# Kernel tuning notes

Hardware: AMD Instinct MI355X
Metric: run time of the kernel (lower is better)

The kernel has to match this reference:

```python
import jax, jax.numpy as jnp
import numpy as np

B, T, C = 8, 1024, 384
L, H, D, F = 8, 16, 24, 1536
EPS = 1e-5

def _ln(x, g, b):
    m = jnp.mean(x, axis=-1, keepdims=True)
    v = jnp.mean(jnp.square(x - m), axis=-1, keepdims=True)
    return (x - m) * jax.lax.rsqrt(v + EPS) * g + b

def setup_inputs() -> dict:
    key = jax.random.key(0)
    ks = jax.random.split(key, 8)
    s = 0.02
    return {
        "idx": jax.random.uniform(ks[0], (B, T, C), jnp.float32),
        "pos_emb": jax.random.normal(ks[1], (T, C), jnp.float32) * s,
        "Wq": jax.random.normal(ks[2], (L, H, C, D), jnp.float32) * s,
        "Wk": jax.random.normal(ks[3], (L, H, C, D), jnp.float32) * s,
        "Wv": jax.random.normal(ks[4], (L, H, C, D), jnp.float32) * s,
        "Wo": jax.random.normal(ks[5], (L, C, C), jnp.float32) * s,
        "bo": jnp.zeros((L, C), jnp.float32),
        "ln1_g": jnp.ones((L, C), jnp.float32),
        "ln1_b": jnp.zeros((L, C), jnp.float32),
        "ln2_g": jnp.ones((L, C), jnp.float32),
        "ln2_b": jnp.zeros((L, C), jnp.float32),
        "W1": jax.random.normal(ks[6], (L, C, F), jnp.float32) * s,
        "b1": jnp.zeros((L, F), jnp.float32),
        "W2": jax.random.normal(ks[7], (L, F, C), jnp.float32) * s,
        "b2": jnp.zeros((L, C), jnp.float32),
        "lnf_g": jnp.ones((C,), jnp.float32),
        "lnf_b": jnp.zeros((C,), jnp.float32),
    }

def reference(idx, pos_emb, Wq, Wk, Wv, Wo, bo, ln1_g, ln1_b, ln2_g, ln2_b,
              W1, b1, W2, b2, lnf_g, lnf_b):
    Bc, Tc, Cc = idx.shape
    x = idx + pos_emb[:Tc]
    causal = jnp.tril(jnp.ones((Tc, Tc), bool))  # [T,T]
    scale = D ** -0.5
    for l in range(L):
        h = _ln(x, ln1_g[l], ln1_b[l])
        q = jnp.einsum('btc,hcd->bhtd', h, Wq[l])
        k = jnp.einsum('btc,hcd->bhtd', h, Wk[l])
        v = jnp.einsum('btc,hcd->bhtd', h, Wv[l])
        wei = jnp.einsum('bhtd,bhsd->bhts', q, k) * scale
        wei = jnp.where(causal, wei, -jnp.inf)
        wei = jax.nn.softmax(wei, axis=-1)
        o = jnp.einsum('bhts,bhsd->bhtd', wei, v)
        o = o.transpose(0, 2, 1, 3).reshape(Bc, Tc, H * D)
        x = x + o @ Wo[l] + bo[l]
        h2 = _ln(x, ln2_g[l], ln2_b[l])
        x = x + jax.nn.relu(h2 @ W1[l] + b1[l]) @ W2[l] + b2[l]
    x = _ln(x, lnf_g, lnf_b)
    return jax.nn.relu(x)  # MSE path with targets=None
```

## Files before the change

kernel.cpp:

```cpp
#include <hip/hip_runtime.h>

#define B_ 8
#define T_ 1024
#define C_ 384
#define L_ 8
#define H_ 16
#define D_ 24
#define F_ 1536
#define M_ 8192

using bf16x8 = __attribute__((ext_vector_type(8))) __bf16;
using f32x4  = __attribute__((ext_vector_type(4))) float;

__device__ __forceinline__ ushort f2b(float f) {
  union { float f; unsigned u; } cv; cv.f = f;
  unsigned u = cv.u;
  return (ushort)((u + 0x7FFFu + ((u >> 16) & 1u)) >> 16);
}
__device__ __forceinline__ ushort f2b_cvt(float f) {
  __bf16 h = (__bf16)f;
  return *(ushort*)&h;
}
__device__ __forceinline__ void gload_lds16(const void* g, void* l) {
  __builtin_amdgcn_global_load_lds((const __attribute__((address_space(1))) void*)g,
                                   (__attribute__((address_space(3))) void*)l, 16, 0, 0);
}

#define QSCL 0.29448870f

__global__ __launch_bounds__(256) void k_embed(const float* __restrict__ idx,
                                               const float* __restrict__ pos,
                                               float* __restrict__ x) {
  long i4 = ((long)blockIdx.x * 256 + threadIdx.x) * 4;
  float4 a = *(const float4*)(idx + i4);
  long p = i4 % (long)(T_ * C_);
  float4 b = *(const float4*)(pos + p);
  a.x += b.x; a.y += b.y; a.z += b.z; a.w += b.w;
  *(float4*)(x + i4) = a;
}

__global__ __launch_bounds__(256) void k_ln(const float* __restrict__ x,
                                            const float* __restrict__ g,
                                            const float* __restrict__ b,
                                            ushort* __restrict__ out) {
  int row  = blockIdx.x * 4 + (threadIdx.x >> 6);
  int lane = threadIdx.x & 63;
  const float* xr = x + (long)row * C_;
  float v[6]; float sum = 0.f;
#pragma unroll
  for (int i = 0; i < 3; ++i) {
    float2 t = *(const float2*)(xr + 2*(lane + 64*i));
    v[2*i] = t.x; v[2*i+1] = t.y; sum += t.x + t.y;
  }
#pragma unroll
  for (int m = 1; m < 64; m <<= 1) sum += __shfl_xor(sum, m);
  float mean = sum * (1.f / C_);
  float vs = 0.f;
#pragma unroll
  for (int i = 0; i < 6; ++i) { float d = v[i] - mean; vs += d * d; }
#pragma unroll
  for (int m = 1; m < 64; m <<= 1) vs += __shfl_xor(vs, m);
  float rstd = rsqrtf(vs * (1.f / C_) + 1e-5f);
  ushort* orow = out + (long)row * C_;
#pragma unroll
  for (int i = 0; i < 3; ++i) {
    int c = 2*(lane + 64*i);
    float2 gg = *(const float2*)(g + c);
    float2 bb = *(const float2*)(b + c);
    ushort2 w;
    w.x = f2b((v[2*i]   - mean) * rstd * gg.x + bb.x);
    w.y = f2b((v[2*i+1] - mean) * rstd * gg.y + bb.y);
    *(ushort2*)(orow + c) = w;
  }
}

__global__ __launch_bounds__(256) void k_lnf(const float* __restrict__ x,
                                             const float* __restrict__ g,
                                             const float* __restrict__ b,
                                             float* __restrict__ out) {
  int row  = blockIdx.x * 4 + (threadIdx.x >> 6);
  int lane = threadIdx.x & 63;
  const float* xr = x + (long)row * C_;
  float v[6]; float sum = 0.f;
#pragma unroll
  for (int i = 0; i < 3; ++i) {
    float2 t = *(const float2*)(xr + 2*(lane + 64*i));
    v[2*i] = t.x; v[2*i+1] = t.y; sum += t.x + t.y;
  }
#pragma unroll
  for (int m = 1; m < 64; m <<= 1) sum += __shfl_xor(sum, m);
  float mean = sum * (1.f / C_);
  float vs = 0.f;
#pragma unroll
  for (int i = 0; i < 6; ++i) { float d = v[i] - mean; vs += d * d; }
#pragma unroll
  for (int m = 1; m < 64; m <<= 1) vs += __shfl_xor(vs, m);
  float rstd = rsqrtf(vs * (1.f / C_) + 1e-5f);
  float* orow = out + (long)row * C_;
#pragma unroll
  for (int i = 0; i < 3; ++i) {
    int c = 2*(lane + 64*i);
    float2 gg = *(const float2*)(g + c);
    float2 bb = *(const float2*)(b + c);
    float2 w;
    w.x = fmaxf((v[2*i]   - mean) * rstd * gg.x + bb.x, 0.f);
    w.y = fmaxf((v[2*i+1] - mean) * rstd * gg.y + bb.y, 0.f);
    *(float2*)(orow + c) = w;
  }
}

__global__ __launch_bounds__(256) void k_trans_qkv(const float* __restrict__ src,
                                                   ushort* __restrict__ dst, int which) {
  __shared__ float tile[32][33];
  int z = blockIdx.z;
  int l = z >> 4, hh = z & 15;
  const float* sb = src + (long)z * C_ * D_;
  ushort* db = dst + (long)l * (3*C_) * C_ + (long)(which * C_ + hh * D_) * C_;
  int r0 = blockIdx.y * 32;
  int tx = threadIdx.x & 31, ty = threadIdx.x >> 5;
#pragma unroll
  for (int i = 0; i < 32; i += 8)
    tile[ty + i][tx] = (tx < D_) ? sb[(long)(r0 + ty + i) * D_ + tx] : 0.f;
  __syncthreads();
#pragma unroll
  for (int i = 0; i < 32; i += 8) {
    int s = ty + i, r = r0 + tx;
    if (s < D_) db[(long)s * C_ + r] = f2b(tile[tx][ty + i]);
  }
}

__global__ __launch_bounds__(256) void k_trans_w(const float* __restrict__ src,
                                                 ushort* __restrict__ dst, int R, int S) {
  __shared__ float tile[32][33];
  const float* sb = src + (long)blockIdx.z * R * S;
  ushort* db = dst + (long)blockIdx.z * R * S;
  int r0 = blockIdx.y * 32, s0 = blockIdx.x * 32;
  int tx = threadIdx.x & 31, ty = threadIdx.x >> 5;
#pragma unroll
  for (int i = 0; i < 32; i += 8) {
    int r = r0 + ty + i, s = s0 + tx;
    tile[ty + i][tx] = (r < R && s < S) ? sb[(long)r * S + s] : 0.f;
  }
  __syncthreads();
#pragma unroll
  for (int i = 0; i < 32; i += 8) {
    int s = s0 + ty + i, r = r0 + tx;
    if (s < S && r < R) db[(long)s * R + r] = f2b(tile[tx][ty + i]);
  }
}

__global__ __launch_bounds__(256) void k_ones(ushort* __restrict__ Vt) {
  ushort4 one4 = {0x3F80, 0x3F80, 0x3F80, 0x3F80};
  *(ushort4*)(Vt + ((long)blockIdx.x * 32 + 24) * 1024 + threadIdx.x * 4) = one4;
}

template<int BN>
__global__ __launch_bounds__(256) void k_gemm(const ushort* __restrict__ A, int lda,
                                              const ushort* __restrict__ Bt, int ldb,
                                              const float* __restrict__ bias,
                                              const float* resid,
                                              float* outF, ushort* outB,
                                              ushort* qp, ushort* kp, ushort* vt,
                                              int N, int K, int relu) {
  __shared__ ushort As[128 * 64];
  __shared__ ushort Bs[BN * 64];
  constexpr int ITB = BN / 32;
  constexpr int MF  = (BN == 128) ? 4 : 2;
  int m0 = blockIdx.y * 128, n0 = blockIdx.x * BN;
  int tid = threadIdx.x, lane = tid & 63, wid = tid >> 6;
  int wr = (BN == 128) ? (wid >> 1) * 64 : wid * 32;
  int wc = (BN == 128) ? (wid & 1) * 64 : 0;
  int g = lane >> 4, q = lane & 15;
  f32x4 acc[MF][4] = {};

  for (int k0 = 0; k0 < K; k0 += 64) {
    __syncthreads();
#pragma unroll
    for (int it = 0; it < 4; ++it) {
      int idx = tid + it * 256;
      int r = idx >> 3;
      int ch = ((idx & 7) ^ (r & 7)) << 3;
      gload_lds16(A + (long)(m0 + r) * lda + k0 + ch,
                  (char*)As + (wid * 64 + it * 256) * 16);
    }
#pragma unroll
    for (int it = 0; it < ITB; ++it) {
      int idx = tid + it * 256;
      int r = idx >> 3;
      int ch = ((idx & 7) ^ (r & 7)) << 3;
      gload_lds16(Bt + (long)(n0 + r) * ldb + k0 + ch,
                  (char*)Bs + (wid * 64 + it * 256) * 16);
    }
    __syncthreads();
#pragma unroll
    for (int kk = 0; kk < 2; ++kk) {
      bf16x8 af[MF], bfr[4];
#pragma unroll
      for (int mi = 0; mi < MF; ++mi) {
        int row = wr + mi * 16 + q;
        int byt = ((row * 64 + kk * 32 + g * 8) * 2) ^ ((row & 7) << 4);
        af[mi] = *(const bf16x8*)((const char*)As + byt);
      }
#pragma unroll
      for (int ni = 0; ni < 4; ++ni) {
        int row = wc + ni * 16 + q;
        int byt = ((row * 64 + kk * 32 + g * 8) * 2) ^ ((row & 7) << 4);
        bfr[ni] = *(const bf16x8*)((const char*)Bs + byt);
      }
#pragma unroll
      for (int mi = 0; mi < MF; ++mi)
#pragma unroll
        for (int ni = 0; ni < 4; ++ni)
          acc[mi][ni] = __builtin_amdgcn_mfma_f32_16x16x32_bf16(af[mi], bfr[ni], acc[mi][ni], 0, 0, 0);
    }
  }
#pragma unroll
  for (int mi = 0; mi < MF; ++mi)
#pragma unroll
    for (int ni = 0; ni < 4; ++ni) {
      int rb = m0 + wr + mi * 16 + g * 4;
      int cc = n0 + wc + ni * 16 + q;
      float bv = bias ? bias[cc] : 0.f;
      float vals[4];
#pragma unroll
      for (int j = 0; j < 4; ++j) {
        float val = acc[mi][ni][j] + bv;
        if (resid) val += resid[(long)(rb + j) * N + cc];
        if (relu)  val = fmaxf(val, 0.f);
        vals[j] = val;
      }
      if (qp) {
        int sec = (cc >= 768) ? 2 : ((cc >= 384) ? 1 : 0);
        int col = cc - sec * 384;
        int hd = (col * 43691) >> 20;
        int dd = col - hd * 24;
        int bb = rb >> 10, tt = rb & 1023;
        int bh = bb * 16 + hd;
        if (sec == 2) {
          ushort4 w4 = { f2b(vals[0]), f2b(vals[1]), f2b(vals[2]), f2b(vals[3]) };
          *(ushort4*)(vt + ((long)bh * 32 + dd) * 1024 + tt) = w4;
        } else {
          float sfac = sec ? 1.f : QSCL;
          ushort* dst = (sec ? kp : qp) + ((long)bh * 1024 + tt) * 32 + dd;
#pragma unroll
          for (int j = 0; j < 4; ++j) dst[j * 32] = f2b(vals[j] * sfac);
        }
      } else {
#pragma unroll
        for (int j = 0; j < 4; ++j) {
          long off = (long)(rb + j) * N + cc;
          if (outF) outF[off] = vals[j];
          if (outB) outB[off] = f2b(vals[j]);
        }
      }
    }
}

__global__ __launch_bounds__(256) void k_attn(const ushort* __restrict__ Qp,
                                              const ushort* __restrict__ Kp,
                                              const ushort* __restrict__ Vt,
                                              ushort* __restrict__ o) {
  __shared__ ushort Ps[4][16][136];
  int bh = blockIdx.x, by = blockIdx.y;
  int b = bh >> 4, hh = bh & 15;
  int tid = threadIdx.x, lane = tid & 63, w = tid >> 6;
  int g = lane >> 4, q = lane & 15;
  const f32x4 zf = {0.f, 0.f, 0.f, 0.f};

  const ushort* qb  = Qp + (long)bh * 1024 * 32;
  const ushort* kb_ = Kp + (long)bh * 1024 * 32;
  const ushort* vtb = Vt + (long)bh * 32 * 1024;

#pragma unroll
  for (int pass = 0; pass < 2; ++pass) {
    int t0 = (pass ? (15 - by) : by) * 64;
    int send = t0 + 64;
    int nT = (send + 127) >> 7;

    bf16x8 qa = *(const bf16x8*)(qb + (t0 + w * 16 + q) * 32 + g * 8);
    f32x4 acc0 = zf, acc1 = zf;

    bf16x8 kf[8];
#pragma unroll
    for (int si = 0; si < 8; ++si)
      kf[si] = *(const bf16x8*)(kb_ + (si * 16 + q) * 32 + g * 8);

    for (int it = 0; it < nT - 1; ++it) {
      int s0 = it << 7;
      f32x4 sc[8];
#pragma unroll
      for (int si = 0; si < 8; ++si)
        sc[si] = __builtin_amdgcn_mfma_f32_16x16x32_bf16(qa, kf[si], zf, 0, 0, 0);
#pragma unroll
      for (int si = 0; si < 8; ++si)
        kf[si] = *(const bf16x8*)(kb_ + (s0 + 128 + si * 16 + q) * 32 + g * 8);
#pragma unroll
      for (int si = 0; si < 8; ++si)
#pragma unroll
        for (int j = 0; j < 4; ++j)
          Ps[w][g * 4 + j][si * 16 + q] = f2b_cvt(exp2f(sc[si][j]));
#pragma unroll
      for (int kk = 0; kk < 4; ++kk) {
        bf16x8 pa  = *(const bf16x8*)(&Ps[w][q][kk * 32 + g * 8]);
        bf16x8 vb0 = *(const bf16x8*)(vtb + (long)q * 1024 + s0 + kk * 32 + g * 8);
        acc0 = __builtin_amdgcn_mfma_f32_16x16x32_bf16(pa, vb0, acc0, 0, 0, 0);
        bf16x8 vb1 = *(const bf16x8*)(vtb + (long)(16 + q) * 1024 + s0 + kk * 32 + g * 8);
        acc1 = __builtin_amdgcn_mfma_f32_16x16x32_bf16(pa, vb1, acc1, 0, 0, 0);
      }
    }
    {
      int s0 = (nT - 1) << 7;
      int rem = send - s0;
      int siMax = rem >> 4, kkMax = rem >> 5;
      f32x4 sc[8];
#pragma unroll
      for (int si = 0; si < 8; ++si)
        if (si < siMax)
          sc[si] = __builtin_amdgcn_mfma_f32_16x16x32_bf16(qa, kf[si], zf, 0, 0, 0);
#pragma unroll
      for (int si = 0; si < 8; ++si)
        if (si < siMax) {
          int s_abs = s0 + si * 16 + q;
#pragma unroll
          for (int j = 0; j < 4; ++j) {
            int t_abs = t0 + w * 16 + g * 4 + j;
            float p = (s_abs <= t_abs) ? exp2f(sc[si][j]) : 0.f;
            Ps[w][g * 4 + j][si * 16 + q] = f2b_cvt(p);
          }
        }
#pragma unroll
      for (int kk = 0; kk < 4; ++kk)
        if (kk < kkMax) {
          bf16x8 pa  = *(const bf16x8*)(&Ps[w][q][kk * 32 + g * 8]);
          bf16x8 vb0 = *(const bf16x8*)(vtb + (long)q * 1024 + s0 + kk * 32 + g * 8);
          acc0 = __builtin_amdgcn_mfma_f32_16x16x32_bf16(pa, vb0, acc0, 0, 0, 0);
          bf16x8 vb1 = *(const bf16x8*)(vtb + (long)(16 + q) * 1024 + s0 + kk * 32 + g * 8);
          acc1 = __builtin_amdgcn_mfma_f32_16x16x32_bf16(pa, vb1, acc1, 0, 0, 0);
        }
    }
    int src = (lane & 48) | 8;
#pragma unroll
    for (int j = 0; j < 4; ++j) {
      float ls = __shfl(acc1[j], src);
      float iv = 1.f / ls;
      int t_abs = t0 + w * 16 + g * 4 + j;
      long orow = (long)(b * T_ + t_abs) * C_ + hh * D_;
      o[orow + q] = f2b(acc0[j] * iv);
      if (q < 8) o[orow + 16 + q] = f2b(acc1[j] * iv);
    }
  }
}

extern "C" void kernel_launch(void* const* d_in, const int* in_sizes, int n_in,
                              void* d_out, int out_size, void* d_ws, size_t ws_size,
                              hipStream_t stream) {
  (void)in_sizes; (void)n_in; (void)out_size; (void)ws_size;
  const float* idx  = (const float*)d_in[0];
  const float* pos  = (const float*)d_in[1];
  const float* Wq   = (const float*)d_in[2];
  const float* Wk   = (const float*)d_in[3];
  const float* Wv   = (const float*)d_in[4];
  const float* Wo   = (const float*)d_in[5];
  const float* bo   = (const float*)d_in[6];
  const float* ln1g = (const float*)d_in[7];
  const float* ln1b = (const float*)d_in[8];
  const float* ln2g = (const float*)d_in[9];
  const float* ln2b = (const float*)d_in[10];
  const float* W1   = (const float*)d_in[11];
  const float* b1   = (const float*)d_in[12];
  const float* W2   = (const float*)d_in[13];
  const float* b2   = (const float*)d_in[14];
  const float* lnfg = (const float*)d_in[15];
  const float* lnfb = (const float*)d_in[16];

  char* ws = (char*)d_ws;
  float*  x     = (float*)(ws);
  ushort* h     = (ushort*)(ws + 12582912);
  ushort* Qp    = (ushort*)(ws + 18874368);
  ushort* Kp    = (ushort*)(ws + 27262976);
  ushort* Vt    = (ushort*)(ws + 35651584);
  ushort* u     = (ushort*)(ws + 44040192);
  ushort* WqkvT = (ushort*)(ws + 69206016);
  ushort* WoT   = (ushort*)(ws + 76283904);
  ushort* W1T   = (ushort*)(ws + 78643200);
  ushort* W2T   = (ushort*)(ws + 88080384);

  hipMemsetAsync(Qp, 0, 25165824, stream);
  k_ones<<<128, 256, 0, stream>>>(Vt);

  k_trans_qkv<<<dim3(1, 12, L_ * H_), 256, 0, stream>>>(Wq, WqkvT, 0);
  k_trans_qkv<<<dim3(1, 12, L_ * H_), 256, 0, stream>>>(Wk, WqkvT, 1);
  k_trans_qkv<<<dim3(1, 12, L_ * H_), 256, 0, stream>>>(Wv, WqkvT, 2);
  k_trans_w<<<dim3(12, 12, L_), 256, 0, stream>>>(Wo, WoT, C_, C_);
  k_trans_w<<<dim3(48, 12, L_), 256, 0, stream>>>(W1, W1T, C_, F_);
  k_trans_w<<<dim3(12, 48, L_), 256, 0, stream>>>(W2, W2T, F_, C_);

  k_embed<<<(M_ * C_) / (256 * 4), 256, 0, stream>>>(idx, pos, x);

  for (int l = 0; l < L_; ++l) {
    k_ln<<<M_ / 4, 256, 0, stream>>>(x, ln1g + l * C_, ln1b + l * C_, h);
    k_gemm<128><<<dim3(1152 / 128, M_ / 128), 256, 0, stream>>>(
        h, C_, WqkvT + (long)l * 1152 * C_, C_,
        nullptr, nullptr, nullptr, nullptr, Qp, Kp, Vt, 1152, C_, 0);
    k_attn<<<dim3(B_ * H_, 8), 256, 0, stream>>>(Qp, Kp, Vt, h);
    k_gemm<64><<<dim3(C_ / 64, M_ / 128), 256, 0, stream>>>(
        h, C_, WoT + (long)l * C_ * C_, C_,
        bo + l * C_, x, x, nullptr, nullptr, nullptr, nullptr, C_, C_, 0);
    k_ln<<<M_ / 4, 256, 0, stream>>>(x, ln2g + l * C_, ln2b + l * C_, h);
    k_gemm<128><<<dim3(F_ / 128, M_ / 128), 256, 0, stream>>>(
        h, C_, W1T + (long)l * F_ * C_, C_,
        b1 + l * F_, nullptr, nullptr, u, nullptr, nullptr, nullptr, F_, C_, 1);
    k_gemm<64><<<dim3(C_ / 64, M_ / 128), 256, 0, stream>>>(
        u, F_, W2T + (long)l * C_ * F_, F_,
        b2 + l * C_, x, x, nullptr, nullptr, nullptr, nullptr, C_, F_, 0);
  }
  k_lnf<<<M_ / 4, 256, 0, stream>>>(x, lnfg, lnfb, (float*)d_out);
}
```

Before: 1.572 ms.

## Keep attention probabilities in registers via transposed QK^T and permuted K layout

The attention kernel now computes S^T (K as the A operand, Q as B), so each lane's score outputs already sit in the MFMA A-operand layout for the P·V product. K rows are written in permuted order by the QKV GEMM epilogue to make this line up. This removes the per-wave LDS round-trip for P and its barrier-free shared stores and loads. Separately, the GEMM is templated on BM, and the N=384 GEMMs use 64x64 tiles to launch twice as many blocks, at the cost of less reuse per tile.

```diff
diff --git a/kernel.cpp b/kernel.cpp
--- a/kernel.cpp
+++ b/kernel.cpp
@@ -21,6 +21,12 @@
   __bf16 h = (__bf16)f;
   return *(ushort*)&h;
 }
+__device__ __forceinline__ unsigned pk2(float a, float b) {
+  union { ushort2 s; unsigned u; } cv;
+  cv.s.x = f2b_cvt(a); cv.s.y = f2b_cvt(b);
+  return cv.u;
+}
+union U4 { uint4 u; bf16x8 v; };
 __device__ __forceinline__ void gload_lds16(const void* g, void* l) {
   __builtin_amdgcn_global_load_lds((const __attribute__((address_space(1))) void*)g,
                                    (__attribute__((address_space(3))) void*)l, 16, 0, 0);
@@ -154,7 +160,7 @@
   *(ushort4*)(Vt + ((long)blockIdx.x * 32 + 24) * 1024 + threadIdx.x * 4) = one4;
 }
 
-template<int BN>
+template<int BM, int BN>
 __global__ __launch_bounds__(256) void k_gemm(const ushort* __restrict__ A, int lda,
                                               const ushort* __restrict__ Bt, int ldb,
                                               const float* __restrict__ bias,
@@ -162,21 +168,23 @@
                                               float* outF, ushort* outB,
                                               ushort* qp, ushort* kp, ushort* vt,
                                               int N, int K, int relu) {
-  __shared__ ushort As[128 * 64];
+  __shared__ ushort As[BM * 64];
   __shared__ ushort Bs[BN * 64];
+  constexpr int ITA = BM / 32;
   constexpr int ITB = BN / 32;
-  constexpr int MF  = (BN == 128) ? 4 : 2;
-  int m0 = blockIdx.y * 128, n0 = blockIdx.x * BN;
+  constexpr int MF_M = BM / 32;
+  constexpr int MF_N = BN / 32;
+  int m0 = blockIdx.y * BM, n0 = blockIdx.x * BN;
   int tid = threadIdx.x, lane = tid & 63, wid = tid >> 6;
-  int wr = (BN == 128) ? (wid >> 1) * 64 : wid * 32;
-  int wc = (BN == 128) ? (wid & 1) * 64 : 0;
+  int wr = (wid >> 1) * (BM / 2);
+  int wc = (wid & 1) * (BN / 2);
   int g = lane >> 4, q = lane & 15;
-  f32x4 acc[MF][4] = {};
+  f32x4 acc[MF_M][MF_N] = {};
 
   for (int k0 = 0; k0 < K; k0 += 64) {
     __syncthreads();
 #pragma unroll
-    for (int it = 0; it < 4; ++it) {
+    for (int it = 0; it < ITA; ++it) {
       int idx = tid + it * 256;
       int r = idx >> 3;
       int ch = ((idx & 7) ^ (r & 7)) << 3;
@@ -194,30 +202,30 @@
     __syncthreads();
 #pragma unroll
     for (int kk = 0; kk < 2; ++kk) {
-      bf16x8 af[MF], bfr[4];
-#pragma unroll
-      for (int mi = 0; mi < MF; ++mi) {
+      bf16x8 af[MF_M], bfr[MF_N];
+#pragma unroll
+      for (int mi = 0; mi < MF_M; ++mi) {
         int row = wr + mi * 16 + q;
         int byt = ((row * 64 + kk * 32 + g * 8) * 2) ^ ((row & 7) << 4);
         af[mi] = *(const bf16x8*)((const char*)As + byt);
       }
 #pragma unroll
-      for (int ni = 0; ni < 4; ++ni) {
+      for (int ni = 0; ni < MF_N; ++ni) {
         int row = wc + ni * 16 + q;
         int byt = ((row * 64 + kk * 32 + g * 8) * 2) ^ ((row & 7) << 4);
         bfr[ni] = *(const bf16x8*)((const char*)Bs + byt);
       }
 #pragma unroll
-      for (int mi = 0; mi < MF; ++mi)
-#pragma unroll
-        for (int ni = 0; ni < 4; ++ni)
+      for (int mi = 0; mi < MF_M; ++mi)
+#pragma unroll
+        for (int ni = 0; ni < MF_N; ++ni)
           acc[mi][ni] = __builtin_amdgcn_mfma_f32_16x16x32_bf16(af[mi], bfr[ni], acc[mi][ni], 0, 0, 0);
     }
   }
 #pragma unroll
-  for (int mi = 0; mi < MF; ++mi)
-#pragma unroll
-    for (int ni = 0; ni < 4; ++ni) {
+  for (int mi = 0; mi < MF_M; ++mi)
+#pragma unroll
+    for (int ni = 0; ni < MF_N; ++ni) {
       int rb = m0 + wr + mi * 16 + g * 4;
       int cc = n0 + wc + ni * 16 + q;
       float bv = bias ? bias[cc] : 0.f;
@@ -241,7 +249,9 @@
           *(ushort4*)(vt + ((long)bh * 32 + dd) * 1024 + tt) = w4;
         } else {
           float sfac = sec ? 1.f : QSCL;
-          ushort* dst = (sec ? kp : qp) + ((long)bh * 1024 + tt) * 32 + dd;
+          int tts = tt;
+          if (sec) tts = (tt & ~31) | ((tt & 4) << 2) | ((tt & 24) >> 1) | (tt & 3);
+          ushort* dst = (sec ? kp : qp) + ((long)bh * 1024 + tts) * 32 + dd;
 #pragma unroll
           for (int j = 0; j < 4; ++j) dst[j * 32] = f2b(vals[j] * sfac);
         }
@@ -260,7 +270,6 @@
                                               const ushort* __restrict__ Kp,
                                               const ushort* __restrict__ Vt,
                                               ushort* __restrict__ o) {
-  __shared__ ushort Ps[4][16][136];
   int bh = blockIdx.x, by = blockIdx.y;
   int b = bh >> 4, hh = bh & 15;
   int tid = threadIdx.x, lane = tid & 63, w = tid >> 6;
@@ -287,55 +296,79 @@
 
     for (int it = 0; it < nT - 1; ++it) {
       int s0 = it << 7;
-      f32x4 sc[8];
-#pragma unroll
-      for (int si = 0; si < 8; ++si)
-        sc[si] = __builtin_amdgcn_mfma_f32_16x16x32_bf16(qa, kf[si], zf, 0, 0, 0);
-#pragma unroll
-      for (int si = 0; si < 8; ++si)
-        kf[si] = *(const bf16x8*)(kb_ + (s0 + 128 + si * 16 + q) * 32 + g * 8);
-#pragma unroll
-      for (int si = 0; si < 8; ++si)
-#pragma unroll
-        for (int j = 0; j < 4; ++j)
-          Ps[w][g * 4 + j][si * 16 + q] = f2b_cvt(exp2f(sc[si][j]));
+      uint4 pa[4];
+      {
+        f32x4 sc[4];
+#pragma unroll
+        for (int si = 0; si < 4; ++si)
+          sc[si] = __builtin_amdgcn_mfma_f32_16x16x32_bf16(kf[si], qa, zf, 0, 0, 0);
+#pragma unroll
+        for (int si = 0; si < 4; ++si)
+          kf[si] = *(const bf16x8*)(kb_ + (s0 + 128 + si * 16 + q) * 32 + g * 8);
+#pragma unroll
+        for (int si = 0; si < 4; ++si) {
+          unsigned d0 = pk2(exp2f(sc[si][0]), exp2f(sc[si][1]));
+          unsigned d1 = pk2(exp2f(sc[si][2]), exp2f(sc[si][3]));
+          if ((si & 1) == 0) { pa[si >> 1].x = d0; pa[si >> 1].y = d1; }
+          else               { pa[si >> 1].z = d0; pa[si >> 1].w = d1; }
+        }
+      }
+      {
+        f32x4 sc[4];
+#pragma unroll
+        for (int si = 0; si < 4; ++si)
+          sc[si] = __builtin_amdgcn_mfma_f32_16x16x32_bf16(kf[si + 4], qa, zf, 0, 0, 0);
+#pragma unroll
+        for (int si = 0; si < 4; ++si)
+          kf[si + 4] = *(const bf16x8*)(kb_ + (s0 + 128 + (si + 4) * 16 + q) * 32 + g * 8);
+#pragma unroll
+        for (int si = 0; si < 4; ++si) {
+          unsigned d0 = pk2(exp2f(sc[si][0]), exp2f(sc[si][1]));
+          unsigned d1 = pk2(exp2f(sc[si][2]), exp2f(sc[si][3]));
+          if ((si & 1) == 0) { pa[2 + (si >> 1)].x = d0; pa[2 + (si >> 1)].y = d1; }
+          else               { pa[2 + (si >> 1)].z = d0; pa[2 + (si >> 1)].w = d1; }
+        }
+      }
 #pragma unroll
       for (int kk = 0; kk < 4; ++kk) {
-        bf16x8 pa  = *(const bf16x8*)(&Ps[w][q][kk * 32 + g * 8]);
+        U4 t; t.u = pa[kk];
         bf16x8 vb0 = *(const bf16x8*)(vtb + (long)q * 1024 + s0 + kk * 32 + g * 8);
-        acc0 = __builtin_amdgcn_mfma_f32_16x16x32_bf16(pa, vb0, acc0, 0, 0, 0);
+        acc0 = __builtin_amdgcn_mfma_f32_16x16x32_bf16(t.v, vb0, acc0, 0, 0, 0);
         bf16x8 vb1 = *(const bf16x8*)(vtb + (long)(16 + q) * 1024 + s0 + kk * 32 + g * 8);
-        acc1 = __builtin_amdgcn_mfma_f32_16x16x32_bf16(pa, vb1, acc1, 0, 0, 0);
+        acc1 = __builtin_amdgcn_mfma_f32_16x16x32_bf16(t.v, vb1, acc1, 0, 0, 0);
       }
     }
     {
       int s0 = (nT - 1) << 7;
       int rem = send - s0;
       int siMax = rem >> 4, kkMax = rem >> 5;
+      uint4 pa[4];
       f32x4 sc[8];
 #pragma unroll
       for (int si = 0; si < 8; ++si)
         if (si < siMax)
-          sc[si] = __builtin_amdgcn_mfma_f32_16x16x32_bf16(qa, kf[si], zf, 0, 0, 0);
+          sc[si] = __builtin_amdgcn_mfma_f32_16x16x32_bf16(kf[si], qa, zf, 0, 0, 0);
+      int t_abs = t0 + w * 16 + q;
 #pragma unroll
       for (int si = 0; si < 8; ++si)
         if (si < siMax) {
-          int s_abs = s0 + si * 16 + q;
-#pragma unroll
-          for (int j = 0; j < 4; ++j) {
-            int t_abs = t0 + w * 16 + g * 4 + j;
-            float p = (s_abs <= t_abs) ? exp2f(sc[si][j]) : 0.f;
-            Ps[w][g * 4 + j][si * 16 + q] = f2b_cvt(p);
-          }
+          int sb = s0 + ((si >> 1) << 5) + ((si & 1) << 2) + (g << 3);
+          float p0 = (sb + 0 <= t_abs) ? exp2f(sc[si][0]) : 0.f;
+          float p1 = (sb + 1 <= t_abs) ? exp2f(sc[si][1]) : 0.f;
+          float p2 = (sb + 2 <= t_abs) ? exp2f(sc[si][2]) : 0.f;
+          float p3 = (sb + 3 <= t_abs) ? exp2f(sc[si][3]) : 0.f;
+          unsigned d0 = pk2(p0, p1), d1 = pk2(p2, p3);
+          if ((si & 1) == 0) { pa[si >> 1].x = d0; pa[si >> 1].y = d1; }
+          else               { pa[si >> 1].z = d0; pa[si >> 1].w = d1; }
         }
 #pragma unroll
       for (int kk = 0; kk < 4; ++kk)
         if (kk < kkMax) {
-          bf16x8 pa  = *(const bf16x8*)(&Ps[w][q][kk * 32 + g * 8]);
+          U4 t; t.u = pa[kk];
           bf16x8 vb0 = *(const bf16x8*)(vtb + (long)q * 1024 + s0 + kk * 32 + g * 8);
-          acc0 = __builtin_amdgcn_mfma_f32_16x16x32_bf16(pa, vb0, acc0, 0, 0, 0);
+          acc0 = __builtin_amdgcn_mfma_f32_16x16x32_bf16(t.v, vb0, acc0, 0, 0, 0);
           bf16x8 vb1 = *(const bf16x8*)(vtb + (long)(16 + q) * 1024 + s0 + kk * 32 + g * 8);
-          acc1 = __builtin_amdgcn_mfma_f32_16x16x32_bf16(pa, vb1, acc1, 0, 0, 0);
+          acc1 = __builtin_amdgcn_mfma_f32_16x16x32_bf16(t.v, vb1, acc1, 0, 0, 0);
         }
     }
     int src = (lane & 48) | 8;
@@ -399,18 +432,18 @@
 
   for (int l = 0; l < L_; ++l) {
     k_ln<<<M_ / 4, 256, 0, stream>>>(x, ln1g + l * C_, ln1b + l * C_, h);
-    k_gemm<128><<<dim3(1152 / 128, M_ / 128), 256, 0, stream>>>(
+    k_gemm<128,128><<<dim3(1152 / 128, M_ / 128), 256, 0, stream>>>(
         h, C_, WqkvT + (long)l * 1152 * C_, C_,
         nullptr, nullptr, nullptr, nullptr, Qp, Kp, Vt, 1152, C_, 0);
     k_attn<<<dim3(B_ * H_, 8), 256, 0, stream>>>(Qp, Kp, Vt, h);
-    k_gemm<64><<<dim3(C_ / 64, M_ / 128), 256, 0, stream>>>(
+    k_gemm<64,64><<<dim3(C_ / 64, M_ / 64), 256, 0, stream>>>(
         h, C_, WoT + (long)l * C_ * C_, C_,
         bo + l * C_, x, x, nullptr, nullptr, nullptr, nullptr, C_, C_, 0);
     k_ln<<<M_ / 4, 256, 0, stream>>>(x, ln2g + l * C_, ln2b + l * C_, h);
-    k_gemm<128><<<dim3(F_ / 128, M_ / 128), 256, 0, stream>>>(
+    k_gemm<128,128><<<dim3(F_ / 128, M_ / 128), 256, 0, stream>>>(
         h, C_, W1T + (long)l * F_ * C_, C_,
         b1 + l * F_, nullptr, nullptr, u, nullptr, nullptr, nullptr, F_, C_, 1);
-    k_gemm<64><<<dim3(C_ / 64, M_ / 128), 256, 0, stream>>>(
+    k_gemm<64,64><<<dim3(C_ / 64, M_ / 64), 256, 0, stream>>>(
         u, F_, W2T + (long)l * C_ * F_, F_,
         b2 + l * C_, x, x, nullptr, nullptr, nullptr, nullptr, C_, F_, 0);
   }
```

Result: no change. 1.568 ms (-0.3%).
